# Kernel optimization log

Hardware: AMD Instinct MI355X
Metric: run time of the kernel (lower is better)

The kernel has to match this reference:

```python
import jax, jax.numpy as jnp
import numpy as np

N = 20000       # nodes
E = 320000      # edges (before self-loops)
F_IN = 128
HID = 128
HEADS = 4
OUT_DIM = 2
B = 64          # graphs in batch
SLOPE = 0.2     # GATv2 leaky_relu negative slope (PyG default)


def _glorot(key, shape):
    fan_in, fan_out = shape[0], shape[1]
    limit = np.sqrt(6.0 / (fan_in + fan_out)).astype(np.float32)
    return jax.random.uniform(key, shape, jnp.float32, -limit, limit)


def setup_inputs() -> dict:
    key = jax.random.key(0)
    ks = jax.random.split(key, 24)
    inp = {
        'x': jax.random.normal(ks[0], (N, F_IN), jnp.float32),
        'edge_src': jax.random.randint(ks[1], (E,), 0, N),
        'edge_dst': jax.random.randint(ks[2], (E,), 0, N),
        'batch': jnp.sort(jax.random.randint(ks[3], (N,), 0, B)),
        # layer 1: in=F_IN, out=HEADS*HID, concat
        'Wl1': _glorot(ks[4], (F_IN, HEADS * HID)),
        'Wr1': _glorot(ks[5], (F_IN, HEADS * HID)),
        'bl1': jnp.zeros((HEADS * HID,), jnp.float32),
        'br1': jnp.zeros((HEADS * HID,), jnp.float32),
        'att1': _glorot(ks[6], (HEADS, HID)),
        'bias1': jnp.zeros((HEADS * HID,), jnp.float32),
        # layer 2: in=HEADS*HID, out=HEADS*HID, concat
        'Wl2': _glorot(ks[7], (HEADS * HID, HEADS * HID)),
        'Wr2': _glorot(ks[8], (HEADS * HID, HEADS * HID)),
        'bl2': jnp.zeros((HEADS * HID,), jnp.float32),
        'br2': jnp.zeros((HEADS * HID,), jnp.float32),
        'att2': _glorot(ks[9], (HEADS, HID)),
        'bias2': jnp.zeros((HEADS * HID,), jnp.float32),
        # layer 3: in=HEADS*HID, heads=1, concat=False -> out=HID
        'Wl3': _glorot(ks[10], (HEADS * HID, HID)),
        'Wr3': _glorot(ks[11], (HEADS * HID, HID)),
        'bl3': jnp.zeros((HID,), jnp.float32),
        'br3': jnp.zeros((HID,), jnp.float32),
        'att3': _glorot(ks[12], (1, HID)),
        'bias3': jnp.zeros((HID,), jnp.float32),
        # output MLP
        'W_mlp1': _glorot(ks[13], (HID, HID)),
        'b_mlp1': jnp.zeros((HID,), jnp.float32),
        'W_mlp2': _glorot(ks[14], (HID, OUT_DIM)),
        'b_mlp2': jnp.zeros((OUT_DIM,), jnp.float32),
    }
    return inp


def gatv2_layer(x, src, dst, Wl, Wr, bl, br, att, bias, concat):
    """PyG GATv2Conv (eval mode): alpha_ij = softmax_j over N(i) of a^T LeakyReLU(xl_j + xr_i)."""
    H, C = att.shape
    n = x.shape[0]
    xl = (x @ Wl + bl).reshape(n, H, C)   # source transform
    e = jax.nn.leaky_relu(xl[src] + (x @ Wr + br).reshape(n, H, C)[dst], SLOPE)  # [E,H,C]
    logits = jnp.einsum('ehc,hc->eh', e, att)                                    # [E,H]
    # segment softmax over destination node
    m = jax.ops.segment_max(logits, dst, num_segments=n)
    alpha = jnp.exp(logits - m[dst])
    denom = jax.ops.segment_sum(alpha, dst, num_segments=n)
    alpha = alpha / denom[dst]
    out = jax.ops.segment_sum(xl[src] * alpha[..., None], dst, num_segments=n)   # [N,H,C]
    out = out.reshape(n, H * C) if concat else out.mean(axis=1)
    return out + bias


def reference(x, edge_src, edge_dst, batch,
              Wl1, Wr1, bl1, br1, att1, bias1,
              Wl2, Wr2, bl2, br2, att2, bias2,
              Wl3, Wr3, bl3, br3, att3, bias3,
              W_mlp1, b_mlp1, W_mlp2, b_mlp2):
    n = x.shape[0]
    loop = jnp.arange(n, dtype=edge_src.dtype)
    src = jnp.concatenate([edge_src, loop])   # PyG add_self_loops=True
    dst = jnp.concatenate([edge_dst, loop])

    h = jax.nn.elu(gatv2_layer(x, src, dst, Wl1, Wr1, bl1, br1, att1, bias1, True))
    h = jax.nn.elu(gatv2_layer(h, src, dst, Wl2, Wr2, bl2, br2, att2, bias2, True))
    h = jax.nn.elu(gatv2_layer(h, src, dst, Wl3, Wr3, bl3, br3, att3, bias3, False))

    # global_mean_pool over graph ids
    counts = jnp.maximum(jax.ops.segment_sum(jnp.ones((n,), h.dtype), batch, num_segments=B), 1.0)
    pooled = jax.ops.segment_sum(h, batch, num_segments=B) / counts[:, None]

    hidden = jax.nn.relu(pooled @ W_mlp1 + b_mlp1)
    return hidden @ W_mlp2 + b_mlp2
```

## Files before the change

kernel.cpp:

```cpp
#include <hip/hip_runtime.h>
#include <math.h>


typedef __attribute__((ext_vector_type(4))) float f32x4;
typedef __attribute__((ext_vector_type(8))) _Float16 f16x8;
typedef __attribute__((ext_vector_type(4))) _Float16 f16x4;
typedef __attribute__((ext_vector_type(2))) _Float16 f16x2;

__device__ __forceinline__ float elu1(float x) {
    return (x > 0.f) ? x : (__expf(x) - 1.f);
}
__device__ __forceinline__ f16x2 pk_leaky(f16x2 s) {
    const f16x2 slope = {(_Float16)0.2f, (_Float16)0.2f};
    return __builtin_elementwise_max(s, s * slope);
}

__device__ __forceinline__ float dpp_sum16(float v) {
    int t;
    t = __builtin_amdgcn_mov_dpp(__float_as_int(v), 0xB1, 0xF, 0xF, true);
    v += __int_as_float(t);
    t = __builtin_amdgcn_mov_dpp(__float_as_int(v), 0x4E, 0xF, 0xF, true);
    v += __int_as_float(t);
    t = __builtin_amdgcn_mov_dpp(__float_as_int(v), 0x141, 0xF, 0xF, true);
    v += __int_as_float(t);
    t = __builtin_amdgcn_mov_dpp(__float_as_int(v), 0x140, 0xF, 0xF, true);
    v += __int_as_float(t);
    return v;
}

__global__ void zero32_kernel(int* __restrict__ p, int n) {
    int i = blockIdx.x * 256 + threadIdx.x;
    if (i < n) p[i] = 0;
}

__global__ void count_kernel(const int* __restrict__ dst, int* __restrict__ cnt,
                             int E, int N) {
    int e = blockIdx.x * 256 + threadIdx.x;
    if (e < E + N) {
        int d = (e < E) ? dst[e] : (e - E);
        atomicAdd(&cnt[d], 1);
    }
}

__global__ __launch_bounds__(256) void scan1_kernel(const int* __restrict__ cnt,
                                                    int* __restrict__ psum, int N) {
    __shared__ int red[256];
    int idx = blockIdx.x * 256 + threadIdx.x;
    red[threadIdx.x] = (idx < N) ? cnt[idx] : 0;
    __syncthreads();
    for (int s = 128; s > 0; s >>= 1) {
        if (threadIdx.x < s) red[threadIdx.x] += red[threadIdx.x + s];
        __syncthreads();
    }
    if (threadIdx.x == 0) psum[blockIdx.x] = red[0];
}
__global__ void scan2_kernel(int* __restrict__ psum, int nch) {
    if (threadIdx.x == 0) {
        int run = 0;
        for (int i = 0; i < nch; ++i) { int v = psum[i]; psum[i] = run; run += v; }
    }
}
__global__ __launch_bounds__(256) void scan3_kernel(const int* __restrict__ cnt,
                                                    const int* __restrict__ psum,
                                                    int* __restrict__ rowstart,
                                                    int* __restrict__ cursor, int N) {
    __shared__ int buf[256];
    int idx = blockIdx.x * 256 + threadIdx.x;
    int v = (idx < N) ? cnt[idx] : 0;
    buf[threadIdx.x] = v;
    __syncthreads();
    for (int off = 1; off < 256; off <<= 1) {
        int t = (threadIdx.x >= off) ? buf[threadIdx.x - off] : 0;
        __syncthreads();
        buf[threadIdx.x] += t;
        __syncthreads();
    }
    int excl = buf[threadIdx.x] - v + psum[blockIdx.x];
    if (idx < N) {
        rowstart[idx] = excl;
        cursor[idx]   = excl;
        if (idx == N - 1) rowstart[N] = excl + v;
    }
}

__global__ void scatter_kernel(const int* __restrict__ src, const int* __restrict__ dst,
                               int* __restrict__ cursor, int* __restrict__ csr_src,
                               int E, int N) {
    int e = blockIdx.x * 256 + threadIdx.x;
    if (e < E + N) {
        int d, s;
        if (e < E) { d = dst[e]; s = src[e]; }
        else       { d = e - E; s = e - E; }
        int pos = atomicAdd(&cursor[d], 1);
        csr_src[pos] = s;
    }
}

__global__ void boundary_kernel(const int* __restrict__ batch,
                                int* __restrict__ gstart, int N, int B) {
    int n = blockIdx.x * 256 + threadIdx.x;
    if (n > N) return;
    int cur  = (n < N) ? batch[n] : B;
    int prev = (n == 0) ? -1 : batch[n - 1];
    for (int g = prev + 1; g <= cur; ++g) gstart[g] = n;
}

__global__ void convA_kernel(const float* __restrict__ X, _Float16* __restrict__ A,
                             int n_valid, int n_total) {
    int i = (blockIdx.x * 256 + threadIdx.x) * 4;
    if (i >= n_total) return;
    float4 v = (i < n_valid) ? *(const float4*)(X + i) : make_float4(0.f, 0.f, 0.f, 0.f);
    f16x4 h;
    h.x = (_Float16)v.x; h.y = (_Float16)v.y;
    h.z = (_Float16)v.z; h.w = (_Float16)v.w;
    *(f16x4*)(A + i) = h;
}

__global__ __launch_bounds__(256) void convWT_kernel(
    const float* __restrict__ Wl, const float* __restrict__ Wr,
    _Float16* __restrict__ Bth, _Float16* __restrict__ Btl, int K, int Nh) {
    __shared__ float tile[32][33];
    int kb = blockIdx.x * 32;
    int nb = blockIdx.y * 32;
    int tx = threadIdx.x;
    int ty = threadIdx.y;
#pragma unroll
    for (int j = 0; j < 4; ++j) {
        int kk = kb + ty + j * 8;
        int nn = nb + tx;
        float v = (nn < Nh) ? Wl[(size_t)kk * Nh + nn]
                            : Wr[(size_t)kk * Nh + (nn - Nh)];
        tile[ty + j * 8][tx] = v;
    }
    __syncthreads();
#pragma unroll
    for (int j = 0; j < 4; ++j) {
        int nn = nb + ty + j * 8;
        int kk = kb + tx;
        float v = tile[tx][ty + j * 8];
        _Float16 h = (_Float16)v;
        Bth[(size_t)nn * K + kk] = h;
        Btl[(size_t)nn * K + kk] = (_Float16)(v - (float)h);
    }
}

#define SCW 132
__global__ __launch_bounds__(256, 1) void gemm_f16_kernel(
    const _Float16* __restrict__ A,
    const _Float16* __restrict__ Bh, const _Float16* __restrict__ Bl,
    const float* __restrict__ biasL, const float* __restrict__ biasR, int Nh_,
    _Float16* __restrict__ P, _Float16* __restrict__ Q, int K, int NT) {
    __shared__ __align__(16) char smem[49152];
    float* sC = (float*)(smem);

    const int tid  = threadIdx.x;
    const int lane = tid & 63;
    const int wv   = tid >> 6;
    const int wm   = wv & 1;
    const int wn   = wv >> 1;
    const int fm   = lane & 15;
    const int q    = lane >> 4;

    const int bi = blockIdx.x;
    const int kx = bi & 7;
    const int tt = bi >> 3;
    const int m0 = ((tt / NT) * 8 + kx) * 128;
    const int n0 = (tt % NT) * 128;

    const int r0  = lane >> 2;
    const int kco = (lane & 3) << 3;

    f32x4 acc[4][4];
#pragma unroll
    for (int i = 0; i < 4; ++i)
#pragma unroll
        for (int j = 0; j < 4; ++j) {
            acc[i][j].x = 0.f; acc[i][j].y = 0.f;
            acc[i][j].z = 0.f; acc[i][j].w = 0.f;
        }

    const int nIters = K >> 5;
    int cur = 0;
    {
        char* base = smem;
#pragma unroll
        for (int j = 0; j < 2; ++j) {
            int wc  = wv * 2 + j;
            int row = wc * 16 + r0;
            size_t ga = (size_t)(m0 + row) * K + kco;
            size_t gb = (size_t)(n0 + row) * K + kco;
            int lofs = wc * 1024;
            __builtin_amdgcn_global_load_lds(
                (const __attribute__((address_space(1))) void*)(A + ga),
                (__attribute__((address_space(3))) void*)(base + lofs), 16, 0, 0);
            __builtin_amdgcn_global_load_lds(
                (const __attribute__((address_space(1))) void*)(Bh + gb),
                (__attribute__((address_space(3))) void*)(base + 8192 + lofs), 16, 0, 0);
            __builtin_amdgcn_global_load_lds(
                (const __attribute__((address_space(1))) void*)(Bl + gb),
                (__attribute__((address_space(3))) void*)(base + 16384 + lofs), 16, 0, 0);
        }
    }
    for (int it = 0; it < nIters; ++it) {
        __syncthreads();
        if (it + 1 < nIters) {
            char* base = smem + (cur ^ 1) * 24576;
            int ks = (it + 1) << 5;
#pragma unroll
            for (int j = 0; j < 2; ++j) {
                int wc  = wv * 2 + j;
                int row = wc * 16 + r0;
                size_t ga = (size_t)(m0 + row) * K + ks + kco;
                size_t gb = (size_t)(n0 + row) * K + ks + kco;
                int lofs = wc * 1024;
                __builtin_amdgcn_global_load_lds(
                    (const __attribute__((address_space(1))) void*)(A + ga),
                    (__attribute__((address_space(3))) void*)(base + lofs), 16, 0, 0);
                __builtin_amdgcn_global_load_lds(
                    (const __attribute__((address_space(1))) void*)(Bh + gb),
                    (__attribute__((address_space(3))) void*)(base + 8192 + lofs), 16, 0, 0);
                __builtin_amdgcn_global_load_lds(
                    (const __attribute__((address_space(1))) void*)(Bl + gb),
                    (__attribute__((address_space(3))) void*)(base + 16384 + lofs), 16, 0, 0);
            }
        }

        _Float16* cA  = (_Float16*)(smem + cur * 24576);
        _Float16* cBh = (_Float16*)(smem + cur * 24576 + 8192);
        _Float16* cBl = (_Float16*)(smem + cur * 24576 + 16384);
        f16x8 ah[4];
#pragma unroll
        for (int mi = 0; mi < 4; ++mi)
            ah[mi] = *(const f16x8*)&cA[(wm * 64 + mi * 16 + fm) * 32 + q * 8];
#pragma unroll
        for (int ni = 0; ni < 4; ++ni) {
            int r = (wn * 64 + ni * 16 + fm) * 32 + q * 8;
            f16x8 bh = *(const f16x8*)&cBh[r];
            f16x8 bl = *(const f16x8*)&cBl[r];
#pragma unroll
            for (int mi = 0; mi < 4; ++mi) {
                acc[mi][ni] = __builtin_amdgcn_mfma_f32_16x16x32_f16(ah[mi], bh, acc[mi][ni], 0, 0, 0);
                acc[mi][ni] = __builtin_amdgcn_mfma_f32_16x16x32_f16(ah[mi], bl, acc[mi][ni], 0, 0, 0);
            }
        }
        cur ^= 1;
    }

    float bsv[4];
#pragma unroll
    for (int ni = 0; ni < 4; ++ni) {
        int col = n0 + wn * 64 + ni * 16 + fm;
        bsv[ni] = (col < Nh_) ? biasL[col] : biasR[col - Nh_];
    }

    _Float16* dstbase = (n0 < Nh_) ? P : Q;
    const int col0 = (n0 < Nh_) ? n0 : (n0 - Nh_);

#pragma unroll
    for (int c = 0; c < 2; ++c) {
        __syncthreads();
        if (wm == c) {
#pragma unroll
            for (int mi = 0; mi < 4; ++mi)
#pragma unroll
                for (int ni = 0; ni < 4; ++ni) {
                    int base = (mi * 16 + q * 4) * SCW + wn * 64 + ni * 16 + fm;
                    sC[base]           = acc[mi][ni].x + bsv[ni];
                    sC[base + SCW]     = acc[mi][ni].y + bsv[ni];
                    sC[base + 2 * SCW] = acc[mi][ni].z + bsv[ni];
                    sC[base + 3 * SCW] = acc[mi][ni].w + bsv[ni];
                }
        }
        __syncthreads();
#pragma unroll
        for (int j = 0; j < 8; ++j) {
            int flat = j * 256 + tid;
            int row  = flat >> 5;
            int col  = (flat & 31) * 4;
            f32x4 v = *(const f32x4*)(sC + row * SCW + col);
            f16x4 hv;
            hv.x = (_Float16)v.x; hv.y = (_Float16)v.y;
            hv.z = (_Float16)v.z; hv.w = (_Float16)v.w;
            *(f16x4*)(dstbase + (size_t)(m0 + c * 64 + row) * Nh_ + col0 + col) = hv;
        }
    }
}


__device__ __forceinline__ void edge4_one(
    int s, const _Float16* __restrict__ P, int c0,
    const f16x2* r2, const f16x2* t2, float& l_run, float* acc) {
    f16x8 h = *(const f16x8*)(P + ((size_t)s << 9) + c0);
    float p = 0.f;
#pragma unroll
    for (int k = 0; k < 4; ++k) {
        f16x2 a; a.x = h[2 * k]; a.y = h[2 * k + 1];
        p = __builtin_amdgcn_fdot2(pk_leaky(a + r2[k]), t2[k], p, false);
    }
    p = dpp_sum16(p);
    float w = __expf(p);
    l_run += w;
#pragma unroll
    for (int j = 0; j < 8; ++j)
        acc[j] = fmaf((float)h[j], w, acc[j]);
}

__global__ __launch_bounds__(256) void gat_edge4_kernel(
    const _Float16* __restrict__ P, const _Float16* __restrict__ Q,
    const float* __restrict__ att, const float* __restrict__ bias,
    const int* __restrict__ rowstart, const int* __restrict__ srcs,
    _Float16* __restrict__ H, int N) {
    int wv = threadIdx.x >> 6;
    int lane = threadIdx.x & 63;
    int n = blockIdx.x * 4 + wv;
    if (n >= N) return;
    int c0 = lane * 8;

    f16x8 rv = *(const f16x8*)(Q + (size_t)n * 512 + c0);
    f16x2 r2[4], t2[4];
#pragma unroll
    for (int k = 0; k < 4; ++k) {
        r2[k].x = rv[2 * k]; r2[k].y = rv[2 * k + 1];
        t2[k].x = (_Float16)att[c0 + 2 * k];
        t2[k].y = (_Float16)att[c0 + 2 * k + 1];
    }

    float acc[8];
#pragma unroll
    for (int j = 0; j < 8; ++j) acc[j] = 0.f;
    float l_run = 0.f;

    int beg = __builtin_amdgcn_readfirstlane(rowstart[n]);
    int end = __builtin_amdgcn_readfirstlane(rowstart[n + 1]);

    int i = beg;
    int s0 = srcs[i], s1 = srcs[i + 1], s2 = srcs[i + 2], s3 = srcs[i + 3];

    for (; i + 3 < end; ) {
        int f0 = srcs[i + 4], f1 = srcs[i + 5], f2 = srcs[i + 6], f3 = srcs[i + 7];
        int u0 = __builtin_amdgcn_readfirstlane(s0);
        int u1 = __builtin_amdgcn_readfirstlane(s1);
        int u2 = __builtin_amdgcn_readfirstlane(s2);
        int u3 = __builtin_amdgcn_readfirstlane(s3);
        f16x8 h0 = *(const f16x8*)(P + ((size_t)u0 << 9) + c0);
        f16x8 h1 = *(const f16x8*)(P + ((size_t)u1 << 9) + c0);
        f16x8 h2 = *(const f16x8*)(P + ((size_t)u2 << 9) + c0);
        f16x8 h3 = *(const f16x8*)(P + ((size_t)u3 << 9) + c0);
        float p0 = 0.f, p1 = 0.f, p2 = 0.f, p3 = 0.f;
#pragma unroll
        for (int k = 0; k < 4; ++k) {
            f16x2 a0; a0.x = h0[2 * k]; a0.y = h0[2 * k + 1];
            f16x2 a1; a1.x = h1[2 * k]; a1.y = h1[2 * k + 1];
            f16x2 a2; a2.x = h2[2 * k]; a2.y = h2[2 * k + 1];
            f16x2 a3; a3.x = h3[2 * k]; a3.y = h3[2 * k + 1];
            p0 = __builtin_amdgcn_fdot2(pk_leaky(a0 + r2[k]), t2[k], p0, false);
            p1 = __builtin_amdgcn_fdot2(pk_leaky(a1 + r2[k]), t2[k], p1, false);
            p2 = __builtin_amdgcn_fdot2(pk_leaky(a2 + r2[k]), t2[k], p2, false);
            p3 = __builtin_amdgcn_fdot2(pk_leaky(a3 + r2[k]), t2[k], p3, false);
        }
        p0 = dpp_sum16(p0);
        p1 = dpp_sum16(p1);
        p2 = dpp_sum16(p2);
        p3 = dpp_sum16(p3);
        float w0 = __expf(p0);
        float w1 = __expf(p1);
        float w2 = __expf(p2);
        float w3 = __expf(p3);
        l_run += (w0 + w1) + (w2 + w3);
#pragma unroll
        for (int j = 0; j < 8; ++j) {
            float a = fmaf((float)h0[j], w0, acc[j]);
            a = fmaf((float)h1[j], w1, a);
            a = fmaf((float)h2[j], w2, a);
            acc[j] = fmaf((float)h3[j], w3, a);
        }
        i += 4; s0 = f0; s1 = f1; s2 = f2; s3 = f3;
    }
    int rem = end - i;
    if (rem > 0) edge4_one(__builtin_amdgcn_readfirstlane(s0), P, c0, r2, t2, l_run, acc);
    if (rem > 1) edge4_one(__builtin_amdgcn_readfirstlane(s1), P, c0, r2, t2, l_run, acc);
    if (rem > 2) edge4_one(__builtin_amdgcn_readfirstlane(s2), P, c0, r2, t2, l_run, acc);

    float inv = 1.f / l_run;
    f16x8 oh;
#pragma unroll
    for (int j = 0; j < 8; ++j)
        oh[j] = (_Float16)elu1(acc[j] * inv + bias[c0 + j]);
    *(f16x8*)(H + (size_t)n * 512 + c0) = oh;
}

__global__ __launch_bounds__(256) void gat_edge1_kernel(
    const _Float16* __restrict__ P, const _Float16* __restrict__ Q,
    const float* __restrict__ att, const float* __restrict__ bias,
    const int* __restrict__ rowstart, const int* __restrict__ srcs,
    float* __restrict__ out, int N) {
    int wv = threadIdx.x >> 6;
    int lane = threadIdx.x & 63;
    int n = blockIdx.x * 4 + wv;
    if (n >= N) return;
    int qd = lane >> 4;
    int lq = lane & 15;
    int c0 = lq * 8;

    f16x8 rv = *(const f16x8*)(Q + (size_t)n * 128 + c0);
    f16x2 r2[4], t2[4];
#pragma unroll
    for (int k = 0; k < 4; ++k) {
        r2[k].x = rv[2 * k]; r2[k].y = rv[2 * k + 1];
        t2[k].x = (_Float16)att[c0 + 2 * k];
        t2[k].y = (_Float16)att[c0 + 2 * k + 1];
    }

    float acc[8];
#pragma unroll
    for (int j = 0; j < 8; ++j) acc[j] = 0.f;
    float l_run = 0.f;

    int beg = __builtin_amdgcn_readfirstlane(rowstart[n]);
    int end = __builtin_amdgcn_readfirstlane(rowstart[n + 1]);
    for (int e = beg + qd; e < end; e += 4) {
        int s = srcs[e];
        f16x8 hv = *(const f16x8*)(P + ((size_t)s << 7) + c0);
        float p = 0.f;
#pragma unroll
        for (int k = 0; k < 4; ++k) {
            f16x2 a; a.x = hv[2 * k]; a.y = hv[2 * k + 1];
            p = __builtin_amdgcn_fdot2(pk_leaky(a + r2[k]), t2[k], p, false);
        }
        p = dpp_sum16(p);
        float w = __expf(p);
        l_run += w;
#pragma unroll
        for (int j = 0; j < 8; ++j)
            acc[j] = fmaf((float)hv[j], w, acc[j]);
    }
    l_run += __shfl_xor(l_run, 16, 64);
    l_run += __shfl_xor(l_run, 32, 64);
#pragma unroll
    for (int j = 0; j < 8; ++j) {
        acc[j] += __shfl_xor(acc[j], 16, 64);
        acc[j] += __shfl_xor(acc[j], 32, 64);
    }
    float inv = 1.f / l_run;
    int cw = c0 + qd * 2;
    float2 w2;
    w2.x = elu1(acc[qd * 2]     * inv + bias[cw]);
    w2.y = elu1(acc[qd * 2 + 1] * inv + bias[cw + 1]);
    *(float2*)(out + (size_t)n * 128 + cw) = w2;
}

__global__ __launch_bounds__(256) void pool2_kernel(
    const float* __restrict__ h3, const int* __restrict__ gstart,
    float* __restrict__ pooled) {
    __shared__ float red[256];
    int g = blockIdx.x;
    int c = threadIdx.x & 127;
    int h = threadIdx.x >> 7;
    int gs = gstart[g], ge = gstart[g + 1];
    float s = 0.f;
    for (int n = gs + h; n < ge; n += 2) s += h3[(size_t)n * 128 + c];
    red[threadIdx.x] = s;
    __syncthreads();
    if (h == 0) {
        float tot = red[c] + red[c + 128];
        float cnt = fmaxf((float)(ge - gs), 1.f);
        pooled[g * 128 + c] = tot / cnt;
    }
}

__global__ __launch_bounds__(128) void mlp_kernel(
    const float* __restrict__ pooled,
    const float* __restrict__ W1, const float* __restrict__ b1,
    const float* __restrict__ W2, const float* __restrict__ b2,
    float* __restrict__ out) {
    __shared__ float pr[128];
    __shared__ float2 red[128];
    int g = blockIdx.x;
    int t = threadIdx.x;
    pr[t] = pooled[g * 128 + t];
    __syncthreads();
    float h = b1[t];
#pragma unroll 4
    for (int k = 0; k < 128; ++k) h = fmaf(pr[k], W1[k * 128 + t], h);
    h = fmaxf(h, 0.0f);
    red[t] = make_float2(h * W2[t * 2], h * W2[t * 2 + 1]);
    __syncthreads();
    for (int s = 64; s > 0; s >>= 1) {
        if (t < s) {
            red[t].x += red[t + s].x;
            red[t].y += red[t + s].y;
        }
        __syncthreads();
    }
    if (t == 0) {
        out[g * 2]     = red[0].x + b2[0];
        out[g * 2 + 1] = red[0].y + b2[1];
    }
}

extern "C" void kernel_launch(void* const* d_in, const int* in_sizes, int n_in,
                              void* d_out, int out_size, void* d_ws, size_t ws_size,
                              hipStream_t stream) {
    const float* x     = (const float*)d_in[0];
    const int*   esrc  = (const int*)d_in[1];
    const int*   edst  = (const int*)d_in[2];
    const int*   batch = (const int*)d_in[3];
    const float* Wl1   = (const float*)d_in[4];
    const float* Wr1   = (const float*)d_in[5];
    const float* bl1   = (const float*)d_in[6];
    const float* br1   = (const float*)d_in[7];
    const float* att1  = (const float*)d_in[8];
    const float* bias1 = (const float*)d_in[9];
    const float* Wl2   = (const float*)d_in[10];
    const float* Wr2   = (const float*)d_in[11];
    const float* bl2   = (const float*)d_in[12];
    const float* br2   = (const float*)d_in[13];
    const float* att2  = (const float*)d_in[14];
    const float* bias2 = (const float*)d_in[15];
    const float* Wl3   = (const float*)d_in[16];
    const float* Wr3   = (const float*)d_in[17];
    const float* bl3   = (const float*)d_in[18];
    const float* br3   = (const float*)d_in[19];
    const float* att3  = (const float*)d_in[20];
    const float* bias3 = (const float*)d_in[21];
    const float* Wm1   = (const float*)d_in[22];
    const float* bm1   = (const float*)d_in[23];
    const float* Wm2   = (const float*)d_in[24];
    const float* bm2   = (const float*)d_in[25];

    int N  = in_sizes[0] / 128;
    int E  = in_sizes[1];
    int ET = E + N;
    int B  = out_size / 2;
    const int Mp = 160 * 128;
    int nch = (N + 255) / 256;

    char* ws = (char*)d_ws;
    size_t off = 0;
    auto alloc = [&](size_t bytes) -> void* {
        void* p = ws + off;
        off += (bytes + 255) & ~(size_t)255;
        return p;
    };
    _Float16* P    = (_Float16*)alloc((size_t)Mp * 512 * 2);
    _Float16* Q    = (_Float16*)alloc((size_t)Mp * 512 * 2);
    _Float16* A1   = (_Float16*)alloc((size_t)Mp * 128 * 2);
    _Float16* Hb   = (_Float16*)alloc((size_t)Mp * 512 * 2);
    _Float16* Wth1 = (_Float16*)alloc((size_t)1024 * 128 * 2);
    _Float16* Wtl1 = (_Float16*)alloc((size_t)1024 * 128 * 2);
    _Float16* Wth2 = (_Float16*)alloc((size_t)1024 * 512 * 2);
    _Float16* Wtl2 = (_Float16*)alloc((size_t)1024 * 512 * 2);
    _Float16* Wth3 = (_Float16*)alloc((size_t)256 * 512 * 2);
    _Float16* Wtl3 = (_Float16*)alloc((size_t)256 * 512 * 2);
    float*    R3   = (float*)alloc((size_t)Mp * 128 * 4);
    int*    cnt      = (int*)alloc((size_t)N * 4);
    int*    psum     = (int*)alloc((size_t)(nch + 1) * 4);
    int*    rowstart = (int*)alloc((size_t)(N + 1) * 4);
    int*    cursor   = (int*)alloc((size_t)N * 4);
    int*    csr_src  = (int*)alloc((size_t)ET * 4 + 32);
    int*    gstart   = (int*)alloc((size_t)(B + 1) * 4);
    float*  pooled   = (float*)alloc((size_t)B * 128 * 4);
    (void)ws_size;

    zero32_kernel<<<(N + 255) / 256, 256, 0, stream>>>(cnt, N);

    count_kernel<<<(ET + 255) / 256, 256, 0, stream>>>(edst, cnt, E, N);
    scan1_kernel<<<nch, 256, 0, stream>>>(cnt, psum, N);
    scan2_kernel<<<1, 64, 0, stream>>>(psum, nch);
    scan3_kernel<<<nch, 256, 0, stream>>>(cnt, psum, rowstart, cursor, N);
    scatter_kernel<<<(ET + 255) / 256, 256, 0, stream>>>(esrc, edst, cursor, csr_src, E, N);
    boundary_kernel<<<(N + 256) / 256, 256, 0, stream>>>(batch, gstart, N, B);

    convWT_kernel<<<dim3(4, 32),  dim3(32, 8), 0, stream>>>(Wl1, Wr1, Wth1, Wtl1, 128, 512);
    convWT_kernel<<<dim3(16, 32), dim3(32, 8), 0, stream>>>(Wl2, Wr2, Wth2, Wtl2, 512, 512);
    convWT_kernel<<<dim3(16, 8),  dim3(32, 8), 0, stream>>>(Wl3, Wr3, Wth3, Wtl3, 512, 128);

    convA_kernel<<<((Mp * 128 / 4) + 255) / 256, 256, 0, stream>>>(x, A1, N * 128, Mp * 128);

    int eblocks = (N + 3) / 4;

    gemm_f16_kernel<<<160 * 8, 256, 0, stream>>>(A1, Wth1, Wtl1, bl1, br1, 512, P, Q, 128, 8);
    gat_edge4_kernel<<<eblocks, 256, 0, stream>>>(P, Q, att1, bias1, rowstart, csr_src, Hb, N);

    gemm_f16_kernel<<<160 * 8, 256, 0, stream>>>(Hb, Wth2, Wtl2, bl2, br2, 512, P, Q, 512, 8);
    gat_edge4_kernel<<<eblocks, 256, 0, stream>>>(P, Q, att2, bias2, rowstart, csr_src, Hb, N);

    gemm_f16_kernel<<<160 * 2, 256, 0, stream>>>(Hb, Wth3, Wtl3, bl3, br3, 128, P, Q, 512, 2);
    gat_edge1_kernel<<<eblocks, 256, 0, stream>>>(P, Q, att3, bias3, rowstart, csr_src, R3, N);

    pool2_kernel<<<B, 256, 0, stream>>>(R3, gstart, pooled);
    mlp_kernel<<<B, 128, 0, stream>>>(pooled, Wm1, bm1, Wm2, bm2, (float*)d_out);
}
```

Measured before the change: 412.2 us.

## Swizzle GEMM LDS layout and software-pipeline edge gathers in GAT kernels

```diff
diff --git a/kernel.cpp b/kernel.cpp
--- a/kernel.cpp
+++ b/kernel.cpp
@@ -160,6 +160,7 @@
     const int wn   = wv >> 1;
     const int fm   = lane & 15;
     const int q    = lane >> 4;
+    const int qa   = q ^ ((fm >> 1) & 3);
 
     const int bi = blockIdx.x;
     const int kx = bi & 7;
@@ -168,7 +169,7 @@
     const int n0 = (tt % NT) * 128;
 
     const int r0  = lane >> 2;
-    const int kco = (lane & 3) << 3;
+    const int kcs = (((lane & 3) ^ ((lane >> 3) & 3)) << 3);
 
     f32x4 acc[4][4];
 #pragma unroll
@@ -187,8 +188,8 @@
         for (int j = 0; j < 2; ++j) {
             int wc  = wv * 2 + j;
             int row = wc * 16 + r0;
-            size_t ga = (size_t)(m0 + row) * K + kco;
-            size_t gb = (size_t)(n0 + row) * K + kco;
+            size_t ga = (size_t)(m0 + row) * K + kcs;
+            size_t gb = (size_t)(n0 + row) * K + kcs;
             int lofs = wc * 1024;
             __builtin_amdgcn_global_load_lds(
                 (const __attribute__((address_space(1))) void*)(A + ga),
@@ -210,8 +211,8 @@
             for (int j = 0; j < 2; ++j) {
                 int wc  = wv * 2 + j;
                 int row = wc * 16 + r0;
-                size_t ga = (size_t)(m0 + row) * K + ks + kco;
-                size_t gb = (size_t)(n0 + row) * K + ks + kco;
+                size_t ga = (size_t)(m0 + row) * K + ks + kcs;
+                size_t gb = (size_t)(n0 + row) * K + ks + kcs;
                 int lofs = wc * 1024;
                 __builtin_amdgcn_global_load_lds(
                     (const __attribute__((address_space(1))) void*)(A + ga),
@@ -231,10 +232,10 @@
         f16x8 ah[4];
 #pragma unroll
         for (int mi = 0; mi < 4; ++mi)
-            ah[mi] = *(const f16x8*)&cA[(wm * 64 + mi * 16 + fm) * 32 + q * 8];
+            ah[mi] = *(const f16x8*)&cA[(wm * 64 + mi * 16 + fm) * 32 + qa * 8];
 #pragma unroll
         for (int ni = 0; ni < 4; ++ni) {
-            int r = (wn * 64 + ni * 16 + fm) * 32 + q * 8;
+            int r = (wn * 64 + ni * 16 + fm) * 32 + qa * 8;
             f16x8 bh = *(const f16x8*)&cBh[r];
             f16x8 bl = *(const f16x8*)&cBl[r];
 #pragma unroll
@@ -287,22 +288,39 @@
 }
 
 
-__device__ __forceinline__ void edge4_one(
-    int s, const _Float16* __restrict__ P, int c0,
-    const f16x2* r2, const f16x2* t2, float& l_run, float* acc) {
-    f16x8 h = *(const f16x8*)(P + ((size_t)s << 9) + c0);
-    float p = 0.f;
+#define LOADP4(s) (*(const f16x8*)(Pb + ((size_t)((unsigned)(s) < um ? (unsigned)(s) : um) << 9)))
+
+__device__ __forceinline__ void edge4_group(
+    const f16x8& h0, const f16x8& h1, const f16x8& h2, const f16x8& h3,
+    int rem, const f16x2* r2, const f16x2* t2, float& l_run, float* acc) {
+    float p0 = 0.f, p1 = 0.f, p2 = 0.f, p3 = 0.f;
 #pragma unroll
     for (int k = 0; k < 4; ++k) {
-        f16x2 a; a.x = h[2 * k]; a.y = h[2 * k + 1];
-        p = __builtin_amdgcn_fdot2(pk_leaky(a + r2[k]), t2[k], p, false);
-    }
-    p = dpp_sum16(p);
-    float w = __expf(p);
-    l_run += w;
-#pragma unroll
-    for (int j = 0; j < 8; ++j)
-        acc[j] = fmaf((float)h[j], w, acc[j]);
+        f16x2 a0; a0.x = h0[2 * k]; a0.y = h0[2 * k + 1];
+        f16x2 a1; a1.x = h1[2 * k]; a1.y = h1[2 * k + 1];
+        f16x2 a2; a2.x = h2[2 * k]; a2.y = h2[2 * k + 1];
+        f16x2 a3; a3.x = h3[2 * k]; a3.y = h3[2 * k + 1];
+        p0 = __builtin_amdgcn_fdot2(pk_leaky(a0 + r2[k]), t2[k], p0, false);
+        p1 = __builtin_amdgcn_fdot2(pk_leaky(a1 + r2[k]), t2[k], p1, false);
+        p2 = __builtin_amdgcn_fdot2(pk_leaky(a2 + r2[k]), t2[k], p2, false);
+        p3 = __builtin_amdgcn_fdot2(pk_leaky(a3 + r2[k]), t2[k], p3, false);
+    }
+    p0 = dpp_sum16(p0);
+    p1 = dpp_sum16(p1);
+    p2 = dpp_sum16(p2);
+    p3 = dpp_sum16(p3);
+    float w0 = __expf(p0);
+    float w1 = (rem > 1) ? __expf(p1) : 0.f;
+    float w2 = (rem > 2) ? __expf(p2) : 0.f;
+    float w3 = (rem > 3) ? __expf(p3) : 0.f;
+    l_run += (w0 + w1) + (w2 + w3);
+#pragma unroll
+    for (int j = 0; j < 8; ++j) {
+        float a = fmaf((float)h0[j], w0, acc[j]);
+        a = fmaf((float)h1[j], w1, a);
+        a = fmaf((float)h2[j], w2, a);
+        acc[j] = fmaf((float)h3[j], w3, a);
+    }
 }
 
 __global__ __launch_bounds__(256) void gat_edge4_kernel(
@@ -315,6 +333,8 @@
     int n = blockIdx.x * 4 + wv;
     if (n >= N) return;
     int c0 = lane * 8;
+    const _Float16* Pb = P + c0;
+    const unsigned um = (unsigned)(N - 1);
 
     f16x8 rv = *(const f16x8*)(Q + (size_t)n * 512 + c0);
     f16x2 r2[4], t2[4];
@@ -332,54 +352,38 @@
 
     int beg = __builtin_amdgcn_readfirstlane(rowstart[n]);
     int end = __builtin_amdgcn_readfirstlane(rowstart[n + 1]);
-
-    int i = beg;
-    int s0 = srcs[i], s1 = srcs[i + 1], s2 = srcs[i + 2], s3 = srcs[i + 3];
-
-    for (; i + 3 < end; ) {
-        int f0 = srcs[i + 4], f1 = srcs[i + 5], f2 = srcs[i + 6], f3 = srcs[i + 7];
-        int u0 = __builtin_amdgcn_readfirstlane(s0);
-        int u1 = __builtin_amdgcn_readfirstlane(s1);
-        int u2 = __builtin_amdgcn_readfirstlane(s2);
-        int u3 = __builtin_amdgcn_readfirstlane(s3);
-        f16x8 h0 = *(const f16x8*)(P + ((size_t)u0 << 9) + c0);
-        f16x8 h1 = *(const f16x8*)(P + ((size_t)u1 << 9) + c0);
-        f16x8 h2 = *(const f16x8*)(P + ((size_t)u2 << 9) + c0);
-        f16x8 h3 = *(const f16x8*)(P + ((size_t)u3 << 9) + c0);
-        float p0 = 0.f, p1 = 0.f, p2 = 0.f, p3 = 0.f;
-#pragma unroll
-        for (int k = 0; k < 4; ++k) {
-            f16x2 a0; a0.x = h0[2 * k]; a0.y = h0[2 * k + 1];
-            f16x2 a1; a1.x = h1[2 * k]; a1.y = h1[2 * k + 1];
-            f16x2 a2; a2.x = h2[2 * k]; a2.y = h2[2 * k + 1];
-            f16x2 a3; a3.x = h3[2 * k]; a3.y = h3[2 * k + 1];
-            p0 = __builtin_amdgcn_fdot2(pk_leaky(a0 + r2[k]), t2[k], p0, false);
-            p1 = __builtin_amdgcn_fdot2(pk_leaky(a1 + r2[k]), t2[k], p1, false);
-            p2 = __builtin_amdgcn_fdot2(pk_leaky(a2 + r2[k]), t2[k], p2, false);
-            p3 = __builtin_amdgcn_fdot2(pk_leaky(a3 + r2[k]), t2[k], p3, false);
-        }
-        p0 = dpp_sum16(p0);
-        p1 = dpp_sum16(p1);
-        p2 = dpp_sum16(p2);
-        p3 = dpp_sum16(p3);
-        float w0 = __expf(p0);
-        float w1 = __expf(p1);
-        float w2 = __expf(p2);
-        float w3 = __expf(p3);
-        l_run += (w0 + w1) + (w2 + w3);
-#pragma unroll
-        for (int j = 0; j < 8; ++j) {
-            float a = fmaf((float)h0[j], w0, acc[j]);
-            a = fmaf((float)h1[j], w1, a);
-            a = fmaf((float)h2[j], w2, a);
-            acc[j] = fmaf((float)h3[j], w3, a);
-        }
-        i += 4; s0 = f0; s1 = f1; s2 = f2; s3 = f3;
-    }
-    int rem = end - i;
-    if (rem > 0) edge4_one(__builtin_amdgcn_readfirstlane(s0), P, c0, r2, t2, l_run, acc);
-    if (rem > 1) edge4_one(__builtin_amdgcn_readfirstlane(s1), P, c0, r2, t2, l_run, acc);
-    if (rem > 2) edge4_one(__builtin_amdgcn_readfirstlane(s2), P, c0, r2, t2, l_run, acc);
+    int cnt = end - beg;
+    int ng  = (cnt + 3) >> 2;
+
+    int sA0 = srcs[beg],     sA1 = srcs[beg + 1];
+    int sA2 = srcs[beg + 2], sA3 = srcs[beg + 3];
+    f16x8 hA0 = LOADP4(sA0), hA1 = LOADP4(sA1);
+    f16x8 hA2 = LOADP4(sA2), hA3 = LOADP4(sA3);
+    int sB0 = srcs[beg + 4], sB1 = srcs[beg + 5];
+    int sB2 = srcs[beg + 6], sB3 = srcs[beg + 7];
+    f16x8 hB0, hB1, hB2, hB3;
+
+    int g = 0;
+    for (;;) {
+        if (g + 1 < ng) {
+            hB0 = LOADP4(sB0); hB1 = LOADP4(sB1);
+            hB2 = LOADP4(sB2); hB3 = LOADP4(sB3);
+        }
+        int nb = beg + (g + 2) * 4;
+        int sC0 = srcs[nb], sC1 = srcs[nb + 1], sC2 = srcs[nb + 2], sC3 = srcs[nb + 3];
+        edge4_group(hA0, hA1, hA2, hA3, cnt - 4 * g, r2, t2, l_run, acc);
+        if (g + 1 >= ng) break;
+
+        if (g + 2 < ng) {
+            hA0 = LOADP4(sC0); hA1 = LOADP4(sC1);
+            hA2 = LOADP4(sC2); hA3 = LOADP4(sC3);
+        }
+        int nb2 = beg + (g + 3) * 4;
+        sB0 = srcs[nb2]; sB1 = srcs[nb2 + 1]; sB2 = srcs[nb2 + 2]; sB3 = srcs[nb2 + 3];
+        edge4_group(hB0, hB1, hB2, hB3, cnt - 4 * (g + 1), r2, t2, l_run, acc);
+        if (g + 2 >= ng) break;
+        g += 2;
+    }
 
     float inv = 1.f / l_run;
     f16x8 oh;
@@ -388,6 +392,8 @@
         oh[j] = (_Float16)elu1(acc[j] * inv + bias[c0 + j]);
     *(f16x8*)(H + (size_t)n * 512 + c0) = oh;
 }
+
+#define LOADP1(s) (*(const f16x8*)(Pb + ((size_t)(s) << 7)))
 
 __global__ __launch_bounds__(256) void gat_edge1_kernel(
     const _Float16* __restrict__ P, const _Float16* __restrict__ Q,
@@ -401,6 +407,7 @@
     int qd = lane >> 4;
     int lq = lane & 15;
     int c0 = lq * 8;
+    const _Float16* Pb = P + c0;
 
     f16x8 rv = *(const f16x8*)(Q + (size_t)n * 128 + c0);
     f16x2 r2[4], t2[4];
@@ -418,22 +425,55 @@
 
     int beg = __builtin_amdgcn_readfirstlane(rowstart[n]);
     int end = __builtin_amdgcn_readfirstlane(rowstart[n + 1]);
-    for (int e = beg + qd; e < end; e += 4) {
-        int s = srcs[e];
-        f16x8 hv = *(const f16x8*)(P + ((size_t)s << 7) + c0);
-        float p = 0.f;
-#pragma unroll
-        for (int k = 0; k < 4; ++k) {
-            f16x2 a; a.x = hv[2 * k]; a.y = hv[2 * k + 1];
-            p = __builtin_amdgcn_fdot2(pk_leaky(a + r2[k]), t2[k], p, false);
-        }
-        p = dpp_sum16(p);
-        float w = __expf(p);
-        l_run += w;
-#pragma unroll
-        for (int j = 0; j < 8; ++j)
-            acc[j] = fmaf((float)hv[j], w, acc[j]);
-    }
+    int cnt = end - beg;
+    int ng  = (cnt + 3) >> 2;
+    int last = end - 1;
+    int e0 = beg + qd;
+
+    int sA = srcs[min(e0, last)];
+    f16x8 hA = LOADP1(sA);
+    int sB = srcs[min(e0 + 4, last)];
+    f16x8 hB;
+
+    int g = 0;
+    for (;;) {
+        if (g + 1 < ng) hB = LOADP1(sB);
+        int sC = srcs[min(e0 + (g + 2) * 4, last)];
+        {
+            float p = 0.f;
+#pragma unroll
+            for (int k = 0; k < 4; ++k) {
+                f16x2 a; a.x = hA[2 * k]; a.y = hA[2 * k + 1];
+                p = __builtin_amdgcn_fdot2(pk_leaky(a + r2[k]), t2[k], p, false);
+            }
+            p = dpp_sum16(p);
+            float w = (e0 + g * 4 < end) ? __expf(p) : 0.f;
+            l_run += w;
+#pragma unroll
+            for (int j = 0; j < 8; ++j)
+                acc[j] = fmaf((float)hA[j], w, acc[j]);
+        }
+        if (g + 1 >= ng) break;
+        if (g + 2 < ng) hA = LOADP1(sC);
+        sB = srcs[min(e0 + (g + 3) * 4, last)];
+        {
+            float p = 0.f;
+#pragma unroll
+            for (int k = 0; k < 4; ++k) {
+                f16x2 a; a.x = hB[2 * k]; a.y = hB[2 * k + 1];
+                p = __builtin_amdgcn_fdot2(pk_leaky(a + r2[k]), t2[k], p, false);
+            }
+            p = dpp_sum16(p);
+            float w = (e0 + (g + 1) * 4 < end) ? __expf(p) : 0.f;
+            l_run += w;
+#pragma unroll
+            for (int j = 0; j < 8; ++j)
+                acc[j] = fmaf((float)hB[j], w, acc[j]);
+        }
+        if (g + 2 >= ng) break;
+        g += 2;
+    }
+
     l_run += __shfl_xor(l_run, 16, 64);
     l_run += __shfl_xor(l_run, 32, 64);
 #pragma unroll
@@ -557,7 +597,7 @@
     int*    psum     = (int*)alloc((size_t)(nch + 1) * 4);
     int*    rowstart = (int*)alloc((size_t)(N + 1) * 4);
     int*    cursor   = (int*)alloc((size_t)N * 4);
-    int*    csr_src  = (int*)alloc((size_t)ET * 4 + 32);
+    int*    csr_src  = (int*)alloc((size_t)ET * 4 + 64);
     int*    gstart   = (int*)alloc((size_t)(B + 1) * 4);
     float*  pooled   = (float*)alloc((size_t)B * 128 * 4);
     (void)ws_size;
```

After: 424.1 us. +2.9%, slower.
